# Optimization experiments

Hardware: AMD Instinct MI355X
Metric: run time of the kernel (lower is better)

Reference implementation:

```python
import jax, jax.numpy as jnp
import numpy as np

D_MODEL = 1024
NUM_HEADS = 16
HEAD_DIM = D_MODEL // NUM_HEADS


def setup_inputs() -> dict:
    key = jax.random.key(0)
    ks = jax.random.split(key, 10)
    B, T, D = 2, 2048, D_MODEL
    scale = 1.0 / np.sqrt(D)
    inp = {
        "x": jax.random.normal(ks[0], (B, T, D), dtype=jnp.float32),
        "mask": jax.random.randint(ks[1], (B, T), 0, 2).astype(jnp.int32),
        "Wq": jax.random.normal(ks[2], (D, D), dtype=jnp.float32) * scale,
        "bq": jnp.zeros((D,), dtype=jnp.float32),
        "Wk": jax.random.normal(ks[3], (D, D), dtype=jnp.float32) * scale,
        "bk": jnp.zeros((D,), dtype=jnp.float32),
        "Wv": jax.random.normal(ks[4], (D, D), dtype=jnp.float32) * scale,
        "bv": jnp.zeros((D,), dtype=jnp.float32),
        "Wo": jax.random.normal(ks[5], (D, D), dtype=jnp.float32) * scale,
        "bo": jnp.zeros((D,), dtype=jnp.float32),
    }
    return inp


def reference(x, mask, Wq, bq, Wk, bk, Wv, bv, Wo, bo):
    B, T, D = x.shape
    H, Hd = NUM_HEADS, HEAD_DIM
    # torch Linear: y = x @ W.T + b
    Q = (x @ Wq.T + bq).reshape(B, T, H, Hd).transpose(0, 2, 1, 3)  # [B,H,T,Hd]
    K = (x @ Wk.T + bk).reshape(B, T, H, Hd).transpose(0, 2, 1, 3)
    V = (x @ Wv.T + bv).reshape(B, T, H, Hd).transpose(0, 2, 1, 3)
    scores = jnp.einsum("bhqd,bhkd->bhqk", Q, K) / jnp.sqrt(jnp.float32(Hd))
    # key padding mask: 1=valid, 0=pad -> -inf on padded keys
    key_pad = (mask == 0)[:, None, None, :]  # [B,1,1,T]
    scores = jnp.where(key_pad, -jnp.inf, scores)
    attn = jax.nn.softmax(scores, axis=-1)  # [B,H,T,T]
    # dropout p=0.0 (inference): identity
    context = jnp.einsum("bhqk,bhkd->bhqd", attn, V)  # [B,H,T,Hd]
    context = context.transpose(0, 2, 1, 3).reshape(B, T, D)
    output = context @ Wo.T + bo
    return (output, attn)
```

## Files before the change

### kernel.cpp

```cpp
#include <hip/hip_runtime.h>
#include <math.h>

#define SEQ   2048
#define BATCH 2
#define DM    1024
#define NH    16
#define HD    64
#define MTOT  (BATCH*SEQ)

typedef __bf16 bf16_t;
typedef __bf16 bf16x4 __attribute__((ext_vector_type(4)));
typedef __bf16 bf16x8 __attribute__((ext_vector_type(8)));
typedef float  f32x4  __attribute__((ext_vector_type(4)));

__global__ __launch_bounds__(256)
void cvt_bf16(const float* __restrict__ in, bf16_t* __restrict__ out, int n)
{
    int i = (blockIdx.x * 256 + threadIdx.x) * 4;
    if (i >= n) return;
    float4 f = *(const float4*)(in + i);
    bf16x4 h;
    h.x = (__bf16)f.x; h.y = (__bf16)f.y; h.z = (__bf16)f.z; h.w = (__bf16)f.w;
    *(bf16x4*)(out + i) = h;
}

template<int MODE>
__global__ __launch_bounds__(256)
void gemm_bt(const bf16_t* __restrict__ A, const bf16_t* __restrict__ W,
             const float* __restrict__ bias, void* __restrict__ outp)
{
    __shared__ __align__(16) bf16_t As[128 * 32];
    __shared__ __align__(16) bf16_t Bs[128 * 32];
    const int n0 = blockIdx.x * 128, m0 = blockIdx.y * 128;
    const int tid = threadIdx.x, lane = tid & 63, wave = tid >> 6;
    const int wm = (wave >> 1) * 64, wn = (wave & 1) * 64;
    const int sr = tid >> 2, sc = (tid & 3) * 8;
    const int fr = lane & 15, fk = (lane >> 4) * 8;
    f32x4 acc[4][4] = {};
    for (int k0 = 0; k0 < DM; k0 += 32) {
        *(uint4*)&As[sr * 32 + sc]        = *(const uint4*)&A[(size_t)(m0 + sr) * DM + k0 + sc];
        *(uint4*)&As[(sr + 64) * 32 + sc] = *(const uint4*)&A[(size_t)(m0 + 64 + sr) * DM + k0 + sc];
        *(uint4*)&Bs[sr * 32 + sc]        = *(const uint4*)&W[(size_t)(n0 + sr) * DM + k0 + sc];
        *(uint4*)&Bs[(sr + 64) * 32 + sc] = *(const uint4*)&W[(size_t)(n0 + 64 + sr) * DM + k0 + sc];
        __syncthreads();
        bf16x8 af[4], bv[4];
        #pragma unroll
        for (int mi = 0; mi < 4; ++mi)
            af[mi] = *(const bf16x8*)&As[(wm + mi * 16 + fr) * 32 + fk];
        #pragma unroll
        for (int ni = 0; ni < 4; ++ni)
            bv[ni] = *(const bf16x8*)&Bs[(wn + ni * 16 + fr) * 32 + fk];
        #pragma unroll
        for (int mi = 0; mi < 4; ++mi)
            #pragma unroll
            for (int ni = 0; ni < 4; ++ni)
                acc[mi][ni] = __builtin_amdgcn_mfma_f32_16x16x32_bf16(af[mi], bv[ni], acc[mi][ni], 0, 0, 0);
        __syncthreads();
    }
    const int cr = (lane >> 4) * 4, cc = lane & 15;
    #pragma unroll
    for (int mi = 0; mi < 4; ++mi) {
        #pragma unroll
        for (int ni = 0; ni < 4; ++ni) {
            const int n = n0 + wn + ni * 16 + cc;
            const float bn = bias[n];
            #pragma unroll
            for (int v = 0; v < 4; ++v) {
                const int m = m0 + wm + mi * 16 + cr + v;
                const float val = acc[mi][ni][v] + bn;
                if (MODE == 0) {
                    const int b_ = m >> 11, t = m & (SEQ - 1);
                    const int h = n >> 6, hd = n & 63;
                    ((bf16_t*)outp)[(((size_t)(b_ * NH + h)) * SEQ + t) * HD + hd] = (__bf16)val;
                } else {
                    ((float*)outp)[(size_t)m * DM + n] = val;
                }
            }
        }
    }
}

__global__ __launch_bounds__(256)
void transpose_v(const bf16_t* __restrict__ Vb, bf16_t* __restrict__ Vt)
{
    const int bh = blockIdx.y, t0 = blockIdx.x * 64;
    __shared__ bf16_t L[64][72];
    const bf16_t* src = Vb + (size_t)bh * SEQ * HD;
    bf16_t* dst = Vt + (size_t)bh * HD * SEQ;
    for (int i = threadIdx.x; i < 64 * 64; i += 256) {
        int r = i >> 6, c = i & 63;
        L[c][r] = src[(size_t)(t0 + r) * HD + c];
    }
    __syncthreads();
    for (int i = threadIdx.x; i < 64 * 64; i += 256) {
        int hd = i >> 6, c = i & 63;
        dst[(size_t)hd * SEQ + t0 + c] = L[hd][c];
    }
}

__global__ __launch_bounds__(256, 2)
void fused_attn(const bf16_t* __restrict__ Q, const bf16_t* __restrict__ K,
                const bf16_t* __restrict__ Vt, const int* __restrict__ mask,
                float* __restrict__ attn, bf16_t* __restrict__ ctxb)
{
    __shared__ __align__(16) bf16_t Qs[2 * 128 * 32];
    __shared__ __align__(16) bf16_t Ks[2 * 128 * 32];
    __shared__ __align__(16) bf16_t Vs[4 * 64 * 32];
    __shared__ __align__(16) bf16_t Ps[4][4 * 32 * 32];

    const int bid = blockIdx.x;
    const int grp = bid & 7, g2 = bid >> 3;
    const int bh = grp * 4 + (g2 >> 4);
    const int qt = g2 & 15;
    const int b = bh >> 4, h = bh & 15;
    const int q0 = qt * 128;

    const bf16_t* Qb  = Q  + (size_t)bh * SEQ * HD;
    const bf16_t* Kb  = K  + (size_t)bh * SEQ * HD;
    const bf16_t* Vtb = Vt + (size_t)bh * HD * SEQ;
    const int*    mb  = mask + b * SEQ;
    float*        Ab  = attn + (size_t)bh * SEQ * SEQ;

    const int tid = threadIdx.x, lane = tid & 63, wave = tid >> 6;
    const int wm = wave * 32;
    const int fr = lane & 15, fg = lane >> 4, fk = fg * 8;
    const int cr = fg * 4, cc = fr;
    const int rsw = ((fr >> 2) & 3) << 3;
    const int wsw = fg << 3;

    {
        const int r = tid >> 2, kq = (tid & 3) * 16;
        #pragma unroll
        for (int rr = 0; rr < 2; ++rr)
            #pragma unroll
            for (int j = 0; j < 2; ++j) {
                const int k = kq + j * 8;
                *(uint4*)&Qs[(k >> 5) * 4096 + (r + rr * 64) * 32 + (k & 31)] =
                    *(const uint4*)&Qb[(size_t)(q0 + r + rr * 64) * HD + k];
            }
    }
    __syncthreads();
    bf16x8 qf[2][2];
    #pragma unroll
    for (int mi = 0; mi < 2; ++mi)
        #pragma unroll
        for (int c = 0; c < 2; ++c)
            qf[mi][c] = *(const bf16x8*)&Qs[c * 4096 + (wm + mi * 16 + fr) * 32 + fk];

    float rm[2][4], rl[2][4];
    #pragma unroll
    for (int mi = 0; mi < 2; ++mi)
        #pragma unroll
        for (int v = 0; v < 4; ++v) { rm[mi][v] = -1e30f; rl[mi][v] = 0.f; }

    for (int kt0 = 0; kt0 < SEQ; kt0 += 128) {
        __syncthreads();
        {
            const int r = tid >> 2, kq = (tid & 3) * 16;
            #pragma unroll
            for (int rr = 0; rr < 2; ++rr)
                #pragma unroll
                for (int j = 0; j < 2; ++j) {
                    const int k = kq + j * 8;
                    *(uint4*)&Ks[(k >> 5) * 4096 + (r + rr * 64) * 32 + (k & 31)] =
                        *(const uint4*)&Kb[(size_t)(kt0 + r + rr * 64) * HD + k];
                }
        }
        __syncthreads();
        float ma[8];
        #pragma unroll
        for (int ni = 0; ni < 8; ++ni)
            ma[ni] = mb[kt0 + ni * 16 + cc] ? 0.f : -1e30f;
        f32x4 acc[2][8] = {};
        #pragma unroll
        for (int ni = 0; ni < 8; ++ni) {
            bf16x8 b0 = *(const bf16x8*)&Ks[(ni * 16 + fr) * 32 + fk];
            bf16x8 b1 = *(const bf16x8*)&Ks[4096 + (ni * 16 + fr) * 32 + fk];
            acc[0][ni] = __builtin_amdgcn_mfma_f32_16x16x32_bf16(qf[0][0], b0, acc[0][ni], 0, 0, 0);
            acc[1][ni] = __builtin_amdgcn_mfma_f32_16x16x32_bf16(qf[1][0], b0, acc[1][ni], 0, 0, 0);
            acc[0][ni] = __builtin_amdgcn_mfma_f32_16x16x32_bf16(qf[0][1], b1, acc[0][ni], 0, 0, 0);
            acc[1][ni] = __builtin_amdgcn_mfma_f32_16x16x32_bf16(qf[1][1], b1, acc[1][ni], 0, 0, 0);
        }
        #pragma unroll
        for (int mi = 0; mi < 2; ++mi) {
            #pragma unroll
            for (int v = 0; v < 4; ++v) {
                float tm = -1e30f;
                #pragma unroll
                for (int ni = 0; ni < 8; ++ni) {
                    float s = acc[mi][ni][v] * 0.125f + ma[ni];
                    acc[mi][ni][v] = s;
                    tm = fmaxf(tm, s);
                }
                tm = fmaxf(tm, __shfl_xor(tm, 1));
                tm = fmaxf(tm, __shfl_xor(tm, 2));
                tm = fmaxf(tm, __shfl_xor(tm, 4));
                tm = fmaxf(tm, __shfl_xor(tm, 8));
                const float mn = fmaxf(rm[mi][v], tm);
                float ls = 0.f;
                #pragma unroll
                for (int ni = 0; ni < 8; ++ni)
                    ls += __expf(acc[mi][ni][v] - mn);
                ls += __shfl_xor(ls, 1);
                ls += __shfl_xor(ls, 2);
                ls += __shfl_xor(ls, 4);
                ls += __shfl_xor(ls, 8);
                rl[mi][v] = rl[mi][v] * __expf(rm[mi][v] - mn) + ls;
                rm[mi][v] = mn;
            }
        }
    }

    float invl[2][4];
    #pragma unroll
    for (int mi = 0; mi < 2; ++mi)
        #pragma unroll
        for (int v = 0; v < 4; ++v)
            invl[mi][v] = 1.0f / rl[mi][v];

    f32x4 oac[2][4] = {};
    bf16_t* Pw = &Ps[wave][0];
    for (int kt0 = 0; kt0 < SEQ; kt0 += 128) {
        __syncthreads();
        {
            const int r = tid >> 2, kq = (tid & 3) * 16;
            #pragma unroll
            for (int rr = 0; rr < 2; ++rr)
                #pragma unroll
                for (int j = 0; j < 2; ++j) {
                    const int k = kq + j * 8;
                    *(uint4*)&Ks[(k >> 5) * 4096 + (r + rr * 64) * 32 + (k & 31)] =
                        *(const uint4*)&Kb[(size_t)(kt0 + r + rr * 64) * HD + k];
                }
        }
        {
            const int hd = tid >> 2, ks = tid & 3;
            #pragma unroll
            for (int j = 0; j < 4; ++j)
                *(uint4*)&Vs[ks * 2048 + hd * 32 + j * 8] =
                    *(const uint4*)&Vtb[(size_t)hd * SEQ + kt0 + ks * 32 + j * 8];
        }
        __syncthreads();
        float ma[8];
        #pragma unroll
        for (int ni = 0; ni < 8; ++ni)
            ma[ni] = mb[kt0 + ni * 16 + cc] ? 0.f : -1e30f;
        f32x4 acc[2][8] = {};
        #pragma unroll
        for (int ni = 0; ni < 8; ++ni) {
            bf16x8 b0 = *(const bf16x8*)&Ks[(ni * 16 + fr) * 32 + fk];
            bf16x8 b1 = *(const bf16x8*)&Ks[4096 + (ni * 16 + fr) * 32 + fk];
            acc[0][ni] = __builtin_amdgcn_mfma_f32_16x16x32_bf16(qf[0][0], b0, acc[0][ni], 0, 0, 0);
            acc[1][ni] = __builtin_amdgcn_mfma_f32_16x16x32_bf16(qf[1][0], b0, acc[1][ni], 0, 0, 0);
            acc[0][ni] = __builtin_amdgcn_mfma_f32_16x16x32_bf16(qf[0][1], b1, acc[0][ni], 0, 0, 0);
            acc[1][ni] = __builtin_amdgcn_mfma_f32_16x16x32_bf16(qf[1][1], b1, acc[1][ni], 0, 0, 0);
        }
        #pragma unroll
        for (int mi = 0; mi < 2; ++mi) {
            #pragma unroll
            for (int ni = 0; ni < 8; ++ni) {
                const int ks = ni >> 1, k2 = (ni & 1) * 16 + cc;
                #pragma unroll
                for (int v = 0; v < 4; ++v) {
                    const int rowl = mi * 16 + cr + v;
                    float s = acc[mi][ni][v] * 0.125f + ma[ni];
                    float p = __expf(s - rm[mi][v]) * invl[mi][v];
                    Ab[(size_t)(q0 + wm + rowl) * SEQ + kt0 + ni * 16 + cc] = p;
                    Pw[(ks * 1024 + rowl * 32 + k2) ^ wsw] = (__bf16)p;
                }
            }
        }
        #pragma unroll
        for (int ks = 0; ks < 4; ++ks) {
            bf16x8 pf[2];
            #pragma unroll
            for (int mi = 0; mi < 2; ++mi)
                pf[mi] = *(const bf16x8*)&Pw[(ks * 1024 + (mi * 16 + fr) * 32 + fk) ^ rsw];
            #pragma unroll
            for (int ni = 0; ni < 4; ++ni) {
                bf16x8 vf = *(const bf16x8*)&Vs[ks * 2048 + (ni * 16 + fr) * 32 + fk];
                oac[0][ni] = __builtin_amdgcn_mfma_f32_16x16x32_bf16(pf[0], vf, oac[0][ni], 0, 0, 0);
                oac[1][ni] = __builtin_amdgcn_mfma_f32_16x16x32_bf16(pf[1], vf, oac[1][ni], 0, 0, 0);
            }
        }
    }
    #pragma unroll
    for (int mi = 0; mi < 2; ++mi) {
        #pragma unroll
        for (int ni = 0; ni < 4; ++ni) {
            #pragma unroll
            for (int v = 0; v < 4; ++v) {
                const int t = q0 + wm + mi * 16 + cr + v;
                ctxb[((size_t)b * SEQ + t) * DM + h * HD + ni * 16 + cc] = (__bf16)oac[mi][ni][v];
            }
        }
    }
}

extern "C" void kernel_launch(void* const* d_in, const int* in_sizes, int n_in,
                              void* d_out, int out_size, void* d_ws, size_t ws_size,
                              hipStream_t stream)
{
    const float* x   = (const float*)d_in[0];
    const int*  mask = (const int*)d_in[1];
    const float* Wq  = (const float*)d_in[2];
    const float* bq  = (const float*)d_in[3];
    const float* Wk  = (const float*)d_in[4];
    const float* bk  = (const float*)d_in[5];
    const float* Wv  = (const float*)d_in[6];
    const float* bv  = (const float*)d_in[7];
    const float* Wo  = (const float*)d_in[8];
    const float* bo  = (const float*)d_in[9];

    float* out  = (float*)d_out;
    float* attn = out + (size_t)BATCH * SEQ * DM;

    const size_t NX = (size_t)MTOT * DM;
    const size_t NW = (size_t)DM * DM;
    const size_t NQ = (size_t)BATCH * NH * SEQ * HD;

    bf16_t* xb   = (bf16_t*)d_ws;
    bf16_t* Wqb  = xb + NX;
    bf16_t* Wkb  = Wqb + NW;
    bf16_t* Wvb  = Wkb + NW;
    bf16_t* Wob  = Wvb + NW;
    bf16_t* Qb   = Wob + NW;
    bf16_t* Kb   = Qb + NQ;
    bf16_t* Vb   = Kb + NQ;
    bf16_t* Vt   = Vb + NQ;
    bf16_t* ctxb = Vt + NQ;

    cvt_bf16<<<dim3(NX / 1024), 256, 0, stream>>>(x, xb, (int)NX);
    cvt_bf16<<<dim3(NW / 1024), 256, 0, stream>>>(Wq, Wqb, (int)NW);
    cvt_bf16<<<dim3(NW / 1024), 256, 0, stream>>>(Wk, Wkb, (int)NW);
    cvt_bf16<<<dim3(NW / 1024), 256, 0, stream>>>(Wv, Wvb, (int)NW);
    cvt_bf16<<<dim3(NW / 1024), 256, 0, stream>>>(Wo, Wob, (int)NW);

    dim3 g1(DM / 128, MTOT / 128);
    gemm_bt<0><<<g1, 256, 0, stream>>>(xb, Wqb, bq, Qb);
    gemm_bt<0><<<g1, 256, 0, stream>>>(xb, Wkb, bk, Kb);
    gemm_bt<0><<<g1, 256, 0, stream>>>(xb, Wvb, bv, Vb);

    transpose_v<<<dim3(SEQ / 64, BATCH * NH), 256, 0, stream>>>(Vb, Vt);

    fused_attn<<<dim3(BATCH * NH * (SEQ / 128)), 256, 0, stream>>>(Qb, Kb, Vt, mask, attn, ctxb);

    gemm_bt<1><<<g1, 256, 0, stream>>>(ctxb, Wob, bo, out);
}
```

Baseline: 820.8 us.

## Fuse QKV projections into one GEMM launch and use direct global-to-LDS loads

Merges the three Q/K/V projection GEMMs into one launch over a 3x-wide N dimension. This relies on Wq, Wk and Wv being contiguous in the workspace, and the bias and output pointers are chosen per column range. The GEMM tile staging now uses global_load_lds to copy global memory directly into shared memory instead of going through registers. This is meant to cut launch overhead, improve occupancy of the projection phase and reduce register and VGPR traffic. It depends on the per-wave LDS layout matching what the MFMA fragment reads expect.

```diff
diff --git a/kernel.cpp b/kernel.cpp
--- a/kernel.cpp
+++ b/kernel.cpp
@@ -7,11 +7,17 @@
 #define NH    16
 #define HD    64
 #define MTOT  (BATCH*SEQ)
+#define NQSZ  ((size_t)BATCH*NH*SEQ*HD)
 
 typedef __bf16 bf16_t;
 typedef __bf16 bf16x4 __attribute__((ext_vector_type(4)));
 typedef __bf16 bf16x8 __attribute__((ext_vector_type(8)));
 typedef float  f32x4  __attribute__((ext_vector_type(4)));
+
+typedef __attribute__((address_space(1))) void glob_void;
+typedef __attribute__((address_space(3))) void lds_void;
+#define GL2LDS(gp, lp) __builtin_amdgcn_global_load_lds( \
+    (glob_void*)(gp), (lds_void*)(lp), 16, 0, 0)
 
 __global__ __launch_bounds__(256)
 void cvt_bf16(const float* __restrict__ in, bf16_t* __restrict__ out, int n)
@@ -27,21 +33,28 @@
 template<int MODE>
 __global__ __launch_bounds__(256)
 void gemm_bt(const bf16_t* __restrict__ A, const bf16_t* __restrict__ W,
-             const float* __restrict__ bias, void* __restrict__ outp)
+             const float* __restrict__ b0p, const float* __restrict__ b1p,
+             const float* __restrict__ b2p, void* __restrict__ outp)
 {
     __shared__ __align__(16) bf16_t As[128 * 32];
     __shared__ __align__(16) bf16_t Bs[128 * 32];
     const int n0 = blockIdx.x * 128, m0 = blockIdx.y * 128;
     const int tid = threadIdx.x, lane = tid & 63, wave = tid >> 6;
     const int wm = (wave >> 1) * 64, wn = (wave & 1) * 64;
-    const int sr = tid >> 2, sc = (tid & 3) * 8;
+    const int srow = wave * 32 + (lane >> 2);
+    const int scol = (lane & 3) * 8;
     const int fr = lane & 15, fk = (lane >> 4) * 8;
+    const bf16_t* gA = &A[(size_t)(m0 + srow) * DM + scol];
+    const bf16_t* gB = &W[(size_t)(n0 + srow) * DM + scol];
+    bf16_t* lA = &As[wave * 1024];
+    bf16_t* lB = &Bs[wave * 1024];
     f32x4 acc[4][4] = {};
     for (int k0 = 0; k0 < DM; k0 += 32) {
-        *(uint4*)&As[sr * 32 + sc]        = *(const uint4*)&A[(size_t)(m0 + sr) * DM + k0 + sc];
-        *(uint4*)&As[(sr + 64) * 32 + sc] = *(const uint4*)&A[(size_t)(m0 + 64 + sr) * DM + k0 + sc];
-        *(uint4*)&Bs[sr * 32 + sc]        = *(const uint4*)&W[(size_t)(n0 + sr) * DM + k0 + sc];
-        *(uint4*)&Bs[(sr + 64) * 32 + sc] = *(const uint4*)&W[(size_t)(n0 + 64 + sr) * DM + k0 + sc];
+        GL2LDS(gA,            lA);
+        GL2LDS(gA + 16 * DM,  lA + 16 * 32);
+        GL2LDS(gB,            lB);
+        GL2LDS(gB + 16 * DM,  lB + 16 * 32);
+        gA += 32; gB += 32;
         __syncthreads();
         bf16x8 af[4], bv[4];
         #pragma unroll
@@ -63,15 +76,24 @@
         #pragma unroll
         for (int ni = 0; ni < 4; ++ni) {
             const int n = n0 + wn + ni * 16 + cc;
-            const float bn = bias[n];
+            float bn;
+            if (MODE == 0) {
+                const int which = n >> 10, nn = n & 1023;
+                const float* bp = which == 0 ? b0p : (which == 1 ? b1p : b2p);
+                bn = bp[nn];
+            } else {
+                bn = b0p[n];
+            }
             #pragma unroll
             for (int v = 0; v < 4; ++v) {
                 const int m = m0 + wm + mi * 16 + cr + v;
                 const float val = acc[mi][ni][v] + bn;
                 if (MODE == 0) {
+                    const int which = n >> 10, nn = n & 1023;
                     const int b_ = m >> 11, t = m & (SEQ - 1);
-                    const int h = n >> 6, hd = n & 63;
-                    ((bf16_t*)outp)[(((size_t)(b_ * NH + h)) * SEQ + t) * HD + hd] = (__bf16)val;
+                    const int h = nn >> 6, hd = nn & 63;
+                    ((bf16_t*)outp)[(size_t)which * NQSZ +
+                        (((size_t)(b_ * NH + h)) * SEQ + t) * HD + hd] = (__bf16)val;
                 } else {
                     ((float*)outp)[(size_t)m * DM + n] = val;
                 }
@@ -317,7 +339,6 @@
 
     const size_t NX = (size_t)MTOT * DM;
     const size_t NW = (size_t)DM * DM;
-    const size_t NQ = (size_t)BATCH * NH * SEQ * HD;
 
     bf16_t* xb   = (bf16_t*)d_ws;
     bf16_t* Wqb  = xb + NX;
@@ -325,10 +346,10 @@
     bf16_t* Wvb  = Wkb + NW;
     bf16_t* Wob  = Wvb + NW;
     bf16_t* Qb   = Wob + NW;
-    bf16_t* Kb   = Qb + NQ;
-    bf16_t* Vb   = Kb + NQ;
-    bf16_t* Vt   = Vb + NQ;
-    bf16_t* ctxb = Vt + NQ;
+    bf16_t* Kb   = Qb + NQSZ;
+    bf16_t* Vb   = Kb + NQSZ;
+    bf16_t* Vt   = Vb + NQSZ;
+    bf16_t* ctxb = Vt + NQSZ;
 
     cvt_bf16<<<dim3(NX / 1024), 256, 0, stream>>>(x, xb, (int)NX);
     cvt_bf16<<<dim3(NW / 1024), 256, 0, stream>>>(Wq, Wqb, (int)NW);
@@ -336,14 +357,11 @@
     cvt_bf16<<<dim3(NW / 1024), 256, 0, stream>>>(Wv, Wvb, (int)NW);
     cvt_bf16<<<dim3(NW / 1024), 256, 0, stream>>>(Wo, Wob, (int)NW);
 
-    dim3 g1(DM / 128, MTOT / 128);
-    gemm_bt<0><<<g1, 256, 0, stream>>>(xb, Wqb, bq, Qb);
-    gemm_bt<0><<<g1, 256, 0, stream>>>(xb, Wkb, bk, Kb);
-    gemm_bt<0><<<g1, 256, 0, stream>>>(xb, Wvb, bv, Vb);
+    gemm_bt<0><<<dim3(3 * DM / 128, MTOT / 128), 256, 0, stream>>>(xb, Wqb, bq, bk, bv, Qb);
 
     transpose_v<<<dim3(SEQ / 64, BATCH * NH), 256, 0, stream>>>(Vb, Vt);
 
     fused_attn<<<dim3(BATCH * NH * (SEQ / 128)), 256, 0, stream>>>(Qb, Kb, Vt, mask, attn, ctxb);
 
-    gemm_bt<1><<<g1, 256, 0, stream>>>(ctxb, Wob, bo, out);
-}
+    gemm_bt<1><<<dim3(DM / 128, MTOT / 128), 256, 0, stream>>>(ctxb, Wob, bo, bo, bo, out);
+}
```

Result: faster. 782.5 us (-4.7%).
